# Performance work log

Measured on AMD Instinct MI355X. Metric: run time of the kernel, lower is better.

The kernel has to match this reference:

```python
import jax, jax.numpy as jnp
import numpy as np

D_MODEL = 256
HEADS = 4
HEAD_DIM = D_MODEL // HEADS  # 64
BN_EPS = 1e-5


def conv1(x, W, b):
    # Conv1d kernel_size=1 == per-position linear: x [B,C,N], W [O,C], b [O]
    return jnp.einsum('oc,bcn->bon', W, x) + b[:, None]


def setup_inputs() -> dict:
    key = jax.random.key(0)
    ks = jax.random.split(key, 12)
    B, N, M = 4, 4096, 4096
    s = 0.02
    return {
        'x': jax.random.normal(ks[0], (B, D_MODEL, N), jnp.float32),
        'source': jax.random.normal(ks[1], (B, D_MODEL, M), jnp.float32),
        'pq_w': jax.random.normal(ks[2], (D_MODEL, D_MODEL), jnp.float32) * s,
        'pq_b': jnp.zeros((D_MODEL,), jnp.float32),
        'pk_w': jax.random.normal(ks[3], (D_MODEL, D_MODEL), jnp.float32) * s,
        'pk_b': jnp.zeros((D_MODEL,), jnp.float32),
        'pv_w': jax.random.normal(ks[4], (D_MODEL, D_MODEL), jnp.float32) * s,
        'pv_b': jnp.zeros((D_MODEL,), jnp.float32),
        'merge_w': jax.random.normal(ks[5], (D_MODEL, D_MODEL), jnp.float32) * s,
        'merge_b': jnp.zeros((D_MODEL,), jnp.float32),
        'mlp1_w': jax.random.normal(ks[6], (2 * D_MODEL, 2 * D_MODEL), jnp.float32) * s,
        'mlp1_b': jax.random.normal(ks[7], (2 * D_MODEL,), jnp.float32) * s,
        'bn_gamma': jnp.ones((2 * D_MODEL,), jnp.float32),
        'bn_beta': jnp.zeros((2 * D_MODEL,), jnp.float32),
        'mlp2_w': jax.random.normal(ks[8], (D_MODEL, 2 * D_MODEL), jnp.float32) * s,
        'mlp2_b': jnp.zeros((D_MODEL,), jnp.float32),  # nn.init.constant_(mlp[-1].bias, 0.0)
    }


def reference(x, source, pq_w, pq_b, pk_w, pk_b, pv_w, pv_b,
              merge_w, merge_b, mlp1_w, mlp1_b, bn_gamma, bn_beta,
              mlp2_w, mlp2_b):
    B = x.shape[0]
    # projections; torch view(B, dim, heads, -1): channels split as (head_dim, heads)
    q = conv1(x, pq_w, pq_b).reshape(B, HEAD_DIM, HEADS, -1)       # [B,d,h,N]
    k = conv1(source, pk_w, pk_b).reshape(B, HEAD_DIM, HEADS, -1)  # [B,d,h,M]
    v = conv1(source, pv_w, pv_b).reshape(B, HEAD_DIM, HEADS, -1)
    scores = jnp.einsum('bdhn,bdhm->bhnm', q, k) / (HEAD_DIM ** 0.5)
    prob = jax.nn.softmax(scores, axis=-1)                          # [B,h,N,M]
    attn_out = jnp.einsum('bhnm,bdhm->bdhn', prob, v).reshape(B, D_MODEL, -1)
    message = conv1(attn_out, merge_w, merge_b)                     # [B,D,N]
    # MLP: conv(512->512) + BatchNorm1d (training-mode batch stats) + ReLU + conv(512->256)
    h = conv1(jnp.concatenate([x, message], axis=1), mlp1_w, mlp1_b)  # [B,2D,N]
    mean = jnp.mean(h, axis=(0, 2), keepdims=True)
    var = jnp.var(h, axis=(0, 2), keepdims=True)  # biased, as torch BN uses for normalization
    h = bn_gamma[:, None] * (h - mean) * jax.lax.rsqrt(var + BN_EPS) + bn_beta[:, None]
    h = jax.nn.relu(h)
    return conv1(h, mlp2_w, mlp2_b)
```

## Files before the change

kernel.cpp:

```cpp
#include <hip/hip_runtime.h>
#include <hip/hip_bf16.h>

#define D_MODEL 256
#define HEADS 4
#define HD 64
#define BATCH 4
#define SEQ 4096
#define NPOS (BATCH*SEQ)
#define SCALE_LOG2 0.18033688011112042f
#define MCHUNKS 2

typedef __attribute__((ext_vector_type(4))) float floatx4;
typedef __attribute__((ext_vector_type(8))) short bf16x8;
typedef __attribute__((ext_vector_type(4))) short bf16x4;
typedef __attribute__((ext_vector_type(4))) unsigned short ushortx4;

__device__ __forceinline__ float bf2f(unsigned short b) {
    return __uint_as_float(((unsigned int)b) << 16);
}
__device__ __forceinline__ unsigned short f2bf(float f) {
    unsigned int u = __float_as_uint(f);
    return (unsigned short)((u + 0x7fffu + ((u >> 16) & 1u)) >> 16);
}
__device__ __forceinline__ bf16x4 pack_bf16x4(float a, float b, float c, float d) {
    __hip_bfloat162 lo = __float22bfloat162_rn(float2{a, b});
    __hip_bfloat162 hi = __float22bfloat162_rn(float2{c, d});
    union { __hip_bfloat162 h2[2]; bf16x4 v; } u;
    u.h2[0] = lo; u.h2[1] = hi;
    return u.v;
}
__device__ __forceinline__ bf16x8 pack_bf16x8(floatx4 a, floatx4 b) {
    union { bf16x4 h[2]; bf16x8 v; } u;
    u.h[0] = pack_bf16x4(a[0], a[1], a[2], a[3]);
    u.h[1] = pack_bf16x4(b[0], b[1], b[2], b[3]);
    return u.v;
}
#define MFMA(a,b,c) __builtin_amdgcn_mfma_f32_16x16x32_bf16((a),(b),(c),0,0,0)
#define EXP2(x) __builtin_amdgcn_exp2f(x)

__global__ __launch_bounds__(256) void prep_all(
        const float* __restrict__ pq_w, const float* __restrict__ pk_w,
        const float* __restrict__ pv_w, const float* __restrict__ merge_w,
        const float* __restrict__ mlp1_w, const float* __restrict__ mlp2_w,
        const float* __restrict__ mlp1_b, const float* __restrict__ merge_b,
        const float* __restrict__ x, const float* __restrict__ src,
        unsigned short* __restrict__ wqb, unsigned short* __restrict__ wkb,
        unsigned short* __restrict__ wvb,
        unsigned short* __restrict__ w1b, unsigned short* __restrict__ w2b,
        unsigned short* __restrict__ xT, unsigned short* __restrict__ srcT,
        unsigned short* __restrict__ w1f, float* __restrict__ b1f,
        float* __restrict__ bn_zero)
{
    __shared__ unsigned short smem[64 * 264];
    const int t = threadIdx.x;
    const int bx = blockIdx.x;
    if (bx < 576) {
        int linear = bx * 1024 + t * 4;
        const float* srcW; unsigned short* dst; int off;
        if (linear < 65536)       { srcW = pq_w;   dst = wqb; off = 0; }
        else if (linear < 131072) { srcW = pk_w;   dst = wkb; off = 65536; }
        else if (linear < 196608) { srcW = pv_w;   dst = wvb; off = 131072; }
        else if (linear < 458752) { srcW = mlp1_w; dst = w1b; off = 196608; }
        else                      { srcW = mlp2_w; dst = w2b; off = 458752; }
        int i = linear - off;
        float4 w = *(const float4*)&srcW[i];
        ushortx4 s = { f2bf(w.x), f2bf(w.y), f2bf(w.z), f2bf(w.w) };
        *(ushortx4*)&dst[i] = s;
        return;
    }
    if (bx < 1088) {
        unsigned short (*lT)[264] = (unsigned short (*)[264])smem;
        int z = bx - 576;
        const float* X = (z < 256) ? x : src;
        unsigned short* O = (z < 256) ? xT : srcT;
        int rem = z & 255;
        int b = rem >> 6, n0 = (rem & 63) * 64;
#pragma unroll
        for (int r = 0; r < 16; ++r) {
            int idx = r * 256 + t;
            int ch = idx >> 4, nnq = (idx & 15) * 4;
            float4 v4 = *(const float4*)&X[((size_t)b * 256 + ch) * SEQ + n0 + nnq];
            lT[nnq + 0][ch] = f2bf(v4.x);
            lT[nnq + 1][ch] = f2bf(v4.y);
            lT[nnq + 2][ch] = f2bf(v4.z);
            lT[nnq + 3][ch] = f2bf(v4.w);
        }
        __syncthreads();
#pragma unroll
        for (int r = 0; r < 8; ++r) {
            int idx = r * 256 + t;
            int row = idx >> 5, cg = (idx & 31) * 8;
            *(bf16x8*)&O[((size_t)b * SEQ + n0 + row) * 256 + cg] = *(const bf16x8*)&lT[row][cg];
        }
        return;
    }
    if (bx < 1104) {
        unsigned short (*lA)[40] = (unsigned short (*)[40])smem;
        unsigned short (*lB)[40] = (unsigned short (*)[40])(smem + 64 * 40);
        const int lane = t & 63, wid = t >> 6;
        const int wm = wid >> 1, wn = wid & 1;
        const int lrow = lane & 15, quad = lane >> 4;
        const int fb = bx - 1088;
        const int c0  = (fb & 1) * 128;
        const int o20 = (fb >> 1) * 64;

        floatx4 acc[2][4];
#pragma unroll
        for (int i = 0; i < 2; ++i)
#pragma unroll
            for (int j = 0; j < 4; ++j) acc[i][j] = (floatx4){0.f,0.f,0.f,0.f};

        for (int k0 = 0; k0 < 256; k0 += 32) {
#pragma unroll
            for (int r = 0; r < 2; ++r) {
                int linear = r * 1024 + t * 4;
                int row = linear >> 5, col = linear & 31;
                float4 w = *(const float4*)&mlp1_w[(size_t)(o20 + row) * 512 + 256 + k0 + col];
                ushortx4 s = { f2bf(w.x), f2bf(w.y), f2bf(w.z), f2bf(w.w) };
                *(ushortx4*)&lA[row][col] = s;
            }
#pragma unroll
            for (int r = 0; r < 2; ++r) {
                int linear = r * 256 + t;
                int row = linear >> 2, cg = (linear & 3) * 8;
                int cp = c0 + row;
                int pc = ((cp & 63) << 2) | (cp >> 6);
                unsigned short s[8];
#pragma unroll
                for (int j = 0; j < 8; ++j)
                    s[j] = f2bf(merge_w[(size_t)(k0 + cg + j) * 256 + pc]);
                *(bf16x8*)&lB[row][cg] = *(const bf16x8*)s;
            }
            __syncthreads();
            bf16x8 aF[2], bF[4];
            const int kq = quad * 8;
#pragma unroll
            for (int mt = 0; mt < 2; ++mt)
                aF[mt] = *(const bf16x8*)&lA[wm*32 + mt*16 + lrow][kq];
#pragma unroll
            for (int nt = 0; nt < 4; ++nt)
                bF[nt] = *(const bf16x8*)&lB[wn*64 + nt*16 + lrow][kq];
#pragma unroll
            for (int mt = 0; mt < 2; ++mt)
#pragma unroll
                for (int nt = 0; nt < 4; ++nt)
                    acc[mt][nt] = MFMA(aF[mt], bF[nt], acc[mt][nt]);
            __syncthreads();
        }
#pragma unroll
        for (int nt = 0; nt < 4; ++nt) {
            int cp = c0 + wn*64 + nt*16 + lrow;
#pragma unroll
            for (int mt = 0; mt < 2; ++mt)
#pragma unroll
                for (int j = 0; j < 4; ++j) {
                    int o2 = o20 + wm*32 + mt*16 + quad*4 + j;
                    w1f[(size_t)o2 * 256 + cp] = f2bf(acc[mt][nt][j]);
                }
        }
        return;
    }
    if (bx < 1106) {
        int o2 = (bx - 1104) * 256 + t;
        float s = mlp1_b[o2];
        for (int o = 0; o < 256; ++o)
            s += mlp1_w[(size_t)o2 * 512 + 256 + o] * merge_b[o];
        b1f[o2] = s;
        return;
    }
    *(float4*)&bn_zero[t * 4] = float4{0.f, 0.f, 0.f, 0.f};
}

__global__ __launch_bounds__(256) void proj_qkv_all(
        const unsigned short* __restrict__ Wq, const float* __restrict__ bq,
        const unsigned short* __restrict__ Wk, const float* __restrict__ bk,
        const unsigned short* __restrict__ Wv, const float* __restrict__ bv,
        const unsigned short* __restrict__ xT, const unsigned short* __restrict__ srcT,
        unsigned short* __restrict__ qo, unsigned short* __restrict__ ko,
        unsigned short* __restrict__ vo)
{
    __shared__ unsigned short smem[2][128 * 80];
    unsigned short (*stage)[72] = (unsigned short (*)[72])&smem[0][0];
    unsigned short* stage2 = &smem[0][0];
    const int t = threadIdx.x;
    const int lane = t & 63, wid = t >> 6;
    const int wm = wid >> 1, wn = wid & 1;
    const int lrow = lane & 15, quad = lane >> 4;
    const int mode = blockIdx.x >> 1;
    const int ob = (blockIdx.x & 1) * 128;
    const int n0 = blockIdx.y * 128;
    const int b  = blockIdx.z;
    const unsigned short* W  = (mode == 0) ? Wq : (mode == 1) ? Wk : Wv;
    const float* bias        = (mode == 0) ? bq : (mode == 1) ? bk : bv;
    const unsigned short* XT = (mode == 0) ? xT : srcT;
    unsigned short* out      = (mode == 0) ? qo : (mode == 1) ? ko : vo;

    const int srow[2] = { (0*256 + t) >> 2, (1*256 + t) >> 2 };
    const int scg = (t & 3) * 8;

    floatx4 acc[4][4];
#pragma unroll
    for (int i = 0; i < 4; ++i)
#pragma unroll
        for (int j = 0; j < 4; ++j) acc[i][j] = (floatx4){0.f,0.f,0.f,0.f};

    bf16x8 rW[2], rX[2];
#pragma unroll
    for (int r = 0; r < 2; ++r) {
        rW[r] = *(const bf16x8*)&W[(size_t)(ob + srow[r]) * 256 + scg];
        rX[r] = *(const bf16x8*)&XT[((size_t)b * SEQ + n0 + srow[r]) * 256 + scg];
    }
#pragma unroll
    for (int r = 0; r < 2; ++r) {
        *(bf16x8*)&smem[0][srow[r]*40 + scg]           = rW[r];
        *(bf16x8*)&smem[0][128*40 + srow[r]*40 + scg]  = rX[r];
    }
    __syncthreads();

    int p = 0;
    for (int kc = 0; kc < 8; ++kc) {
        const bool pre = (kc + 1 < 8);
        if (pre) {
            const int k1 = (kc + 1) * 32;
#pragma unroll
            for (int r = 0; r < 2; ++r) {
                rW[r] = *(const bf16x8*)&W[(size_t)(ob + srow[r]) * 256 + k1 + scg];
                rX[r] = *(const bf16x8*)&XT[((size_t)b * SEQ + n0 + srow[r]) * 256 + k1 + scg];
            }
        }
        bf16x8 aF[4], bF[4];
        const int kq = quad * 8;
#pragma unroll
        for (int mt = 0; mt < 4; ++mt)
            aF[mt] = *(const bf16x8*)&smem[p][(wm*64 + mt*16 + lrow)*40 + kq];
#pragma unroll
        for (int nt = 0; nt < 4; ++nt)
            bF[nt] = *(const bf16x8*)&smem[p][128*40 + (wn*64 + nt*16 + lrow)*40 + kq];
#pragma unroll
        for (int mt = 0; mt < 4; ++mt)
#pragma unroll
            for (int nt = 0; nt < 4; ++nt)
                acc[mt][nt] = MFMA(aF[mt], bF[nt], acc[mt][nt]);
        if (pre) {
#pragma unroll
            for (int r = 0; r < 2; ++r) {
                *(bf16x8*)&smem[p^1][srow[r]*40 + scg]          = rW[r];
                *(bf16x8*)&smem[p^1][128*40 + srow[r]*40 + scg] = rX[r];
            }
        }
        __syncthreads();
        p ^= 1;
    }
    const float osc = (mode == 0) ? SCALE_LOG2 : 1.0f;
    if (mode == 2) {
        for (int half = 0; half < 2; ++half) {
            __syncthreads();
            if (wm == half) {
#pragma unroll
                for (int mt = 0; mt < 4; ++mt)
#pragma unroll
                    for (int j = 0; j < 4; ++j) {
                        int ol = mt*16 + quad*4 + j;
                        float bvv = bias[ob + half*64 + ol];
#pragma unroll
                        for (int nt = 0; nt < 4; ++nt) {
                            int n = wn*64 + nt*16 + lrow;
                            stage2[ol*132 + n] = f2bf(acc[mt][nt][j] + bvv);
                        }
                    }
            }
            __syncthreads();
#pragma unroll
            for (int i = 0; i < 4; ++i) {
                int c = i * 256 + t;
                int row = c >> 4, sub = c & 15;
                int o = ob + half*64 + row;
                int d = o >> 2, h = o & 3;
                *(bf16x8*)&out[((size_t)(b*HEADS + h) * HD + d) * SEQ + n0 + sub*8] =
                    *(const bf16x8*)&stage2[row*132 + sub*8];
            }
        }
        return;
    }
    for (int half = 0; half < 2; ++half) {
        __syncthreads();
        if (wm == half) {
#pragma unroll
            for (int mt = 0; mt < 4; ++mt)
#pragma unroll
                for (int j = 0; j < 4; ++j) {
                    int o = ob + half*64 + mt*16 + quad*4 + j;
                    float bvv = bias[o];
                    int col = j*16 + mt*4 + quad;
#pragma unroll
                    for (int nt = 0; nt < 4; ++nt) {
                        int n = wn*64 + nt*16 + lrow;
                        stage[n][col] = f2bf((acc[mt][nt][j] + bvv) * osc);
                    }
                }
        }
        __syncthreads();
#pragma unroll
        for (int i = 0; i < 4; ++i) {
            int c = i * 256 + t;
            int n = c >> 3, h = (c >> 1) & 3, sub = c & 1;
            bf16x8 val = *(const bf16x8*)&stage[n][h*16 + sub*8];
            int d0 = (ob >> 2) + half*16 + sub*8;
            *(bf16x8*)&out[((size_t)(b*HEADS + h) * SEQ + n0 + n) * HD + d0] = val;
        }
    }
}

__global__ __launch_bounds__(256, 2) void flash_attn(
        const unsigned short* __restrict__ q,
        const unsigned short* __restrict__ k,
        const unsigned short* __restrict__ v,
        unsigned short* __restrict__ poO, float* __restrict__ pol)
{
    __shared__ unsigned short smem[2][9216];
    const int t = threadIdx.x, lane = t & 63, wid = t >> 6;
    const int lrow = lane & 15, quad = lane >> 4;
    const int bc = blockIdx.x, qt = blockIdx.y;
    const int bh = bc & 15, chunk = bc >> 4;
    const int hb = (bh & 3) * BATCH + (bh >> 2);
    const int r0 = qt * 256 + wid * 64;

    bf16x8 qf[4][2];
#pragma unroll
    for (int nh = 0; nh < 4; ++nh) {
        const size_t base = ((size_t)bh * SEQ + r0 + nh*16 + lrow) * HD;
        qf[nh][0] = *(const bf16x8*)&q[base + quad * 8];
        qf[nh][1] = *(const bf16x8*)&q[base + 32 + quad * 8];
    }
    bf16x8 ones;
#pragma unroll
    for (int i = 0; i < 8; ++i) ones[i] = (short)0x3F80;
    int mmv[2], cgv[2], krv[2];
#pragma unroll
    for (int r = 0; r < 2; ++r) {
        int linear = r * 256 + t;
        int mm = linear >> 3, cg = (linear & 7) * 8;
        int c2 = mm >> 5, mp = mm & 31;
        mmv[r] = mm; cgv[r] = cg;
        krv[r] = (c2 << 5) + ((mp & 4) << 2) + ((mp >> 3) << 2) + (mp & 3);
    }
    const size_t kbase = ((size_t)bh * SEQ + chunk * (SEQ/MCHUNKS));
    const size_t vbase = (size_t)bh * HD;
    const int moff = chunk * (SEQ/MCHUNKS);
    const int NIT = SEQ / MCHUNKS / 64;

    floatx4 oacc[4][4], oaccL[4];
#pragma unroll
    for (int nh = 0; nh < 4; ++nh) {
        oaccL[nh] = (floatx4){0.f,0.f,0.f,0.f};
#pragma unroll
        for (int i = 0; i < 4; ++i) oacc[nh][i] = (floatx4){0.f,0.f,0.f,0.f};
    }

    {
        bf16x8 pk[2], pv[2];
#pragma unroll
        for (int r = 0; r < 2; ++r) {
            pk[r] = *(const bf16x8*)&k[(kbase + mmv[r]) * HD + cgv[r]];
            pv[r] = *(const bf16x8*)&v[(vbase + mmv[r]) * SEQ + moff + cgv[r]];
        }
#pragma unroll
        for (int r = 0; r < 2; ++r) {
            *(bf16x8*)&smem[0][krv[r]*72 + cgv[r]]        = pk[r];
            *(bf16x8*)&smem[0][4608 + mmv[r]*72 + cgv[r]] = pv[r];
        }
    }
    __syncthreads();

    int p = 0;
#pragma unroll 1
    for (int it = 0; it < NIT; ++it) {
        bf16x8 pk[2], pv[2];
        const bool pre = (it + 1 < NIT);
        if (pre) {
            const int m1 = (it + 1) * 64;
#pragma unroll
            for (int r = 0; r < 2; ++r) {
                pk[r] = *(const bf16x8*)&k[(kbase + m1 + mmv[r]) * HD + cgv[r]];
                pv[r] = *(const bf16x8*)&v[(vbase + mmv[r]) * SEQ + moff + m1 + cgv[r]];
            }
        }
        const unsigned short* lS = smem[p];

#pragma unroll
        for (int c2 = 0; c2 < 2; ++c2) {
            floatx4 sa[2][4];
#pragma unroll
            for (int AB = 0; AB < 2; ++AB)
#pragma unroll
                for (int nh = 0; nh < 4; ++nh)
                    sa[AB][nh] = (floatx4){0.f,0.f,0.f,0.f};
            __builtin_amdgcn_s_setprio(1);
#pragma unroll
            for (int AB = 0; AB < 2; ++AB) {
#pragma unroll
                for (int kc = 0; kc < 2; ++kc) {
                    bf16x8 kf = *(const bf16x8*)&lS[(c2*32 + AB*16 + lrow)*72 + kc*32 + quad*8];
#pragma unroll
                    for (int nh = 0; nh < 4; ++nh)
                        sa[AB][nh] = MFMA(kf, qf[nh][kc], sa[AB][nh]);
                }
            }
            __builtin_amdgcn_s_setprio(0);
            bf16x8 pf8[4];
#pragma unroll
            for (int nh = 0; nh < 4; ++nh) {
                floatx4 ea, eb;
#pragma unroll
                for (int i = 0; i < 4; ++i) { ea[i] = EXP2(sa[0][nh][i]); eb[i] = EXP2(sa[1][nh][i]); }
                pf8[nh] = pack_bf16x8(ea, eb);
            }
            __builtin_amdgcn_s_setprio(1);
#pragma unroll
            for (int nh = 0; nh < 4; ++nh)
                oaccL[nh] = MFMA(ones, pf8[nh], oaccL[nh]);
#pragma unroll
            for (int dt = 0; dt < 4; ++dt) {
                bf16x8 vf = *(const bf16x8*)&lS[4608 + (dt*16 + lrow)*72 + c2*32 + quad*8];
#pragma unroll
                for (int nh = 0; nh < 4; ++nh)
                    oacc[nh][dt] = MFMA(vf, pf8[nh], oacc[nh][dt]);
            }
            __builtin_amdgcn_s_setprio(0);
        }
        if (pre) {
#pragma unroll
            for (int r = 0; r < 2; ++r) {
                *(bf16x8*)&smem[p^1][krv[r]*72 + cgv[r]]        = pk[r];
                *(bf16x8*)&smem[p^1][4608 + mmv[r]*72 + cgv[r]] = pv[r];
            }
        }
        __syncthreads();
        p ^= 1;
    }
    const size_t prow = (size_t)(chunk*16 + hb) * SEQ + qt * 256;
    if (lane < 16) {
#pragma unroll
        for (int nh = 0; nh < 4; ++nh)
            pol[prow + wid*64 + nh*16 + lrow] = oaccL[nh][0];
    }
    unsigned short* stB = (unsigned short*)&smem[0][0];
#pragma unroll
    for (int nh = 0; nh < 4; ++nh)
#pragma unroll
        for (int dt = 0; dt < 4; ++dt) {
            bf16x4 pv4 = pack_bf16x4(oacc[nh][dt][0], oacc[nh][dt][1],
                                     oacc[nh][dt][2], oacc[nh][dt][3]);
            *(bf16x4*)&stB[(wid*64 + nh*16 + lrow)*72 + dt*16 + quad*4] = pv4;
        }
    __syncthreads();
#pragma unroll
    for (int i = 0; i < 8; ++i) {
        int c = i * 256 + t;
        int row = c >> 3, sub = c & 7;
        *(bf16x8*)&poO[(prow + row) * HD + sub*8] = *(const bf16x8*)&stB[row*72 + sub*8];
    }
}

__global__ __launch_bounds__(256) void gemm_mlp1(
        const unsigned short* __restrict__ xT, const unsigned short* __restrict__ poO,
        const float* __restrict__ pol,
        const unsigned short* __restrict__ w1b, const unsigned short* __restrict__ w1f,
        const float* __restrict__ b1f, unsigned short* __restrict__ h1,
        float* __restrict__ sums, float* __restrict__ sumsq)
{
    __shared__ unsigned short lA[2][64][40];
    __shared__ unsigned short lB[2][128][40];
    __shared__ float sInv[256];
    const int t = threadIdx.x;
    const int lane = t & 63, wid = t >> 6;
    const int wm = wid >> 1, wn = wid & 1;
    const int lrow = lane & 15, quad = lane >> 4;
    const int o0 = blockIdx.x * 128;
    const int p0 = blockIdx.y * 64;
    const int b = p0 >> 12, n0 = p0 & (SEQ - 1);
    const size_t CH = (size_t)16 * SEQ * HD;

    {
        int h = t >> 6, nn = t & 63;
        int hb = h * BATCH + b;
        float l = 0.f;
#pragma unroll
        for (int c = 0; c < MCHUNKS; ++c)
            l += pol[((size_t)(c*16 + hb)) * SEQ + n0 + nn];
        sInv[t] = 1.0f / l;
    }
    __syncthreads();

    const int arow = t >> 2, acg = (t & 3) * 8;
    const int brow[2] = { (0*256 + t) >> 2, (1*256 + t) >> 2 };

    floatx4 acc[2][4];
#pragma unroll
    for (int i = 0; i < 2; ++i)
#pragma unroll
        for (int j = 0; j < 4; ++j) acc[i][j] = (floatx4){0.f,0.f,0.f,0.f};

    bf16x8 rA, rB[2];
    auto load_tile = [&](int k0) {
        if (k0 < 256) {
            rA = *(const bf16x8*)&xT[(size_t)(p0 + arow) * 256 + k0 + acg];
#pragma unroll
            for (int r = 0; r < 2; ++r)
                rB[r] = *(const bf16x8*)&w1b[(size_t)(o0 + brow[r]) * 512 + k0 + acg];
        } else {
            const int kk2 = k0 - 256;
            const int h = kk2 >> 6, d0 = kk2 & 63, hb = h * BATCH + b;
            const unsigned short* bse = &poO[((size_t)hb * SEQ + n0 + arow) * HD + d0 + acg];
            float inv = sInv[h*64 + arow];
            float fs[8];
#pragma unroll
            for (int i = 0; i < 8; ++i) fs[i] = 0.f;
#pragma unroll
            for (int c = 0; c < MCHUNKS; ++c) {
                bf16x8 a = *(const bf16x8*)(bse + (size_t)c * CH);
#pragma unroll
                for (int i = 0; i < 8; ++i)
                    fs[i] += bf2f((unsigned short)a[i]);
            }
            unsigned short res[8];
#pragma unroll
            for (int i = 0; i < 8; ++i)
                res[i] = f2bf(fs[i] * inv);
            rA = *(const bf16x8*)res;
#pragma unroll
            for (int r = 0; r < 2; ++r)
                rB[r] = *(const bf16x8*)&w1f[(size_t)(o0 + brow[r]) * 256 + kk2 + acg];
        }
    };

    load_tile(0);
    *(bf16x8*)&lA[0][arow][acg] = rA;
#pragma unroll
    for (int r = 0; r < 2; ++r) *(bf16x8*)&lB[0][brow[r]][acg] = rB[r];
    __syncthreads();

    int p = 0;
    for (int kc = 0; kc < 16; ++kc) {
        const bool pre = (kc + 1 < 16);
        if (pre) load_tile((kc + 1) * 32);
        bf16x8 aF[2], bF[4];
        const int kq = quad * 8;
#pragma unroll
        for (int mt = 0; mt < 2; ++mt)
            aF[mt] = *(const bf16x8*)&lA[p][wm*32 + mt*16 + lrow][kq];
#pragma unroll
        for (int nt = 0; nt < 4; ++nt)
            bF[nt] = *(const bf16x8*)&lB[p][wn*64 + nt*16 + lrow][kq];
#pragma unroll
        for (int mt = 0; mt < 2; ++mt)
#pragma unroll
            for (int nt = 0; nt < 4; ++nt)
                acc[mt][nt] = MFMA(aF[mt], bF[nt], acc[mt][nt]);
        if (pre) {
            *(bf16x8*)&lA[p^1][arow][acg] = rA;
#pragma unroll
            for (int r = 0; r < 2; ++r) *(bf16x8*)&lB[p^1][brow[r]][acg] = rB[r];
        }
        __syncthreads();
        p ^= 1;
    }
#pragma unroll
    for (int nt = 0; nt < 4; ++nt) {
        int o = o0 + wn*64 + nt*16 + lrow;
        float bvv = b1f[o];
        float s = 0.f, qs = 0.f;
#pragma unroll
        for (int mt = 0; mt < 2; ++mt)
#pragma unroll
            for (int j = 0; j < 4; ++j) {
                int pos = p0 + wm*32 + mt*16 + quad*4 + j;
                float val = acc[mt][nt][j] + bvv;
                h1[(size_t)pos * 512 + o] = f2bf(val);
                s += val; qs += val * val;
            }
        s  += __shfl_xor(s, 16);  s  += __shfl_xor(s, 32);
        qs += __shfl_xor(qs, 16); qs += __shfl_xor(qs, 32);
        if (lane < 16) {
            atomicAdd(&sums[o], s);
            atomicAdd(&sumsq[o], qs);
        }
    }
}

__global__ __launch_bounds__(256) void gemm_mlp2(
        const unsigned short* __restrict__ W2, const unsigned short* __restrict__ h1,
        const float* __restrict__ bias,
        const float* __restrict__ sums, const float* __restrict__ sumsq,
        const float* __restrict__ gamma, const float* __restrict__ beta,
        float* __restrict__ out)
{
    __shared__ unsigned short lA[2][128][40];
    __shared__ unsigned short lB[2][64][40];
    __shared__ float sSc[512], sSh[512];
    const int t = threadIdx.x;
    const int lane = t & 63, wid = t >> 6;
    const int wm = wid >> 1, wn = wid & 1;
    const int lrow = lane & 15, quad = lane >> 4;
    const int o0 = blockIdx.x * 128;
    const int p0 = blockIdx.y * 64;

#pragma unroll
    for (int cc = 0; cc < 2; ++cc) {
        int c = cc * 256 + t;
        float mean = sums[c] * (1.0f / NPOS);
        float var  = sumsq[c] * (1.0f / NPOS) - mean * mean;
        float sc = gamma[c] * rsqrtf(var + 1e-5f);
        sSc[c] = sc;
        sSh[c] = beta[c] - mean * sc;
    }
    __syncthreads();

    const int arow[2] = { (0*256 + t) >> 2, (1*256 + t) >> 2 };
    const int acg = (t & 3) * 8;
    const int brow = t >> 2;

    floatx4 acc[4][2];
#pragma unroll
    for (int i = 0; i < 4; ++i)
#pragma unroll
        for (int j = 0; j < 2; ++j) acc[i][j] = (floatx4){0.f,0.f,0.f,0.f};

    bf16x8 rW[2], rH;
    auto load_tile = [&](int k0) {
#pragma unroll
        for (int r = 0; r < 2; ++r)
            rW[r] = *(const bf16x8*)&W2[(size_t)(o0 + arow[r]) * 512 + k0 + acg];
        bf16x8 hv = *(const bf16x8*)&h1[(size_t)(p0 + brow) * 512 + k0 + acg];
        unsigned short res[8];
#pragma unroll
        for (int i = 0; i < 8; ++i) {
            int c = k0 + acg + i;
            float f = bf2f((unsigned short)hv[i]);
            f = fmaxf(f * sSc[c] + sSh[c], 0.f);
            res[i] = f2bf(f);
        }
        rH = *(const bf16x8*)res;
    };

    load_tile(0);
#pragma unroll
    for (int r = 0; r < 2; ++r) *(bf16x8*)&lA[0][arow[r]][acg] = rW[r];
    *(bf16x8*)&lB[0][brow][acg] = rH;
    __syncthreads();

    int p = 0;
    for (int kc = 0; kc < 16; ++kc) {
        const bool pre = (kc + 1 < 16);
        if (pre) load_tile((kc + 1) * 32);
        bf16x8 aF[4], bF[2];
        const int kq = quad * 8;
#pragma unroll
        for (int mt = 0; mt < 4; ++mt)
            aF[mt] = *(const bf16x8*)&lA[p][wm*64 + mt*16 + lrow][kq];
#pragma unroll
        for (int nt = 0; nt < 2; ++nt)
            bF[nt] = *(const bf16x8*)&lB[p][wn*32 + nt*16 + lrow][kq];
#pragma unroll
        for (int mt = 0; mt < 4; ++mt)
#pragma unroll
            for (int nt = 0; nt < 2; ++nt)
                acc[mt][nt] = MFMA(aF[mt], bF[nt], acc[mt][nt]);
        if (pre) {
#pragma unroll
            for (int r = 0; r < 2; ++r) *(bf16x8*)&lA[p^1][arow[r]][acg] = rW[r];
            *(bf16x8*)&lB[p^1][brow][acg] = rH;
        }
        __syncthreads();
        p ^= 1;
    }
#pragma unroll
    for (int mt = 0; mt < 4; ++mt)
#pragma unroll
        for (int j = 0; j < 4; ++j) {
            int o = o0 + wm*64 + mt*16 + quad*4 + j;
            float bvv = bias[o];
#pragma unroll
            for (int nt = 0; nt < 2; ++nt) {
                int pos = p0 + wn*32 + nt*16 + lrow;
                int b = pos >> 12, n = pos & (SEQ - 1);
                out[((size_t)b * D_MODEL + o) * SEQ + n] = acc[mt][nt][j] + bvv;
            }
        }
}

extern "C" void kernel_launch(void* const* d_in, const int* in_sizes, int n_in,
                              void* d_out, int out_size, void* d_ws, size_t ws_size,
                              hipStream_t stream)
{
    (void)in_sizes; (void)n_in; (void)out_size; (void)ws_size;
    const float* x        = (const float*)d_in[0];
    const float* source   = (const float*)d_in[1];
    const float* pq_w     = (const float*)d_in[2];
    const float* pq_b     = (const float*)d_in[3];
    const float* pk_w     = (const float*)d_in[4];
    const float* pk_b     = (const float*)d_in[5];
    const float* pv_w     = (const float*)d_in[6];
    const float* pv_b     = (const float*)d_in[7];
    const float* merge_w  = (const float*)d_in[8];
    const float* merge_b  = (const float*)d_in[9];
    const float* mlp1_w   = (const float*)d_in[10];
    const float* mlp1_b   = (const float*)d_in[11];
    const float* bn_gamma = (const float*)d_in[12];
    const float* bn_beta  = (const float*)d_in[13];
    const float* mlp2_w   = (const float*)d_in[14];
    const float* mlp2_b   = (const float*)d_in[15];
    float* out = (float*)d_out;

    char* ws = (char*)d_ws;
    const size_t MB = 1ull << 20;
    unsigned short* xT   = (unsigned short*)(ws);
    unsigned short* srcT = (unsigned short*)(ws + 8*MB);
    unsigned short* q    = (unsigned short*)(ws + 16*MB);
    unsigned short* kk   = (unsigned short*)(ws + 24*MB);
    unsigned short* v    = (unsigned short*)(ws + 32*MB);
    unsigned short* poO  = (unsigned short*)(ws + 40*MB);
    unsigned short* h1   = (unsigned short*)(ws + 16*MB);
    float* pol = (float*)(ws + 72*MB);
    unsigned short* wqb = (unsigned short*)(ws + 73*MB);
    unsigned short* wkb = wqb + 65536;
    unsigned short* wvb = wkb + 65536;
    unsigned short* w1b = wvb + 65536;
    unsigned short* w2b = w1b + 262144;
    unsigned short* w1f = w2b + 131072;
    float* b1f = (float*)(w1f + 131072);
    float* bn_sum = b1f + 512;
    float* bn_sumsq = bn_sum + 512;

    prep_all<<<dim3(1107), 256, 0, stream>>>(
        pq_w, pk_w, pv_w, merge_w, mlp1_w, mlp2_w, mlp1_b, merge_b, x, source,
        wqb, wkb, wvb, w1b, w2b, xT, srcT, w1f, b1f, bn_sum);
    proj_qkv_all<<<dim3(6, SEQ/128, BATCH), 256, 0, stream>>>(
        wqb, pq_b, wkb, pk_b, wvb, pv_b, xT, srcT, q, kk, v);
    flash_attn<<<dim3(16*MCHUNKS, SEQ/256), 256, 0, stream>>>(q, kk, v, poO, pol);
    gemm_mlp1<<<dim3(4, NPOS/64), 256, 0, stream>>>(
        xT, poO, pol, w1b, w1f, b1f, h1, bn_sum, bn_sumsq);
    gemm_mlp2<<<dim3(2, NPOS/64), 256, 0, stream>>>(
        w2b, h1, mlp2_b, bn_sum, bn_sumsq, bn_gamma, bn_beta, out);
}
```

Measured before the change: 243.4 us.

## Enlarge mlp1 GEMM tiles, interleave attention chunk partials, parallelize bias fold

gemm_mlp1 now uses 512-thread blocks with 128x256 output tiles instead of 64x128. This quarters the number of blocks, increases operand reuse from shared memory, and halves the BN-stat atomics by reducing across warps in shared memory first. The flash-attention partial outputs and row sums are now stored with the chunk index innermost, so mlp1 reads both chunks contiguously. The bias-folding prep block is spread over 16 blocks with a shuffle reduction instead of 2 blocks doing serial 256-length dot products. The larger tiles cost more registers and LDS per block, which may lower occupancy, and there are fewer blocks (256) to fill the GPU.

```diff
diff --git a/kernel.cpp b/kernel.cpp
--- a/kernel.cpp
+++ b/kernel.cpp
@@ -160,12 +160,15 @@
         }
         return;
     }
-    if (bx < 1106) {
-        int o2 = (bx - 1104) * 256 + t;
-        float s = mlp1_b[o2];
-        for (int o = 0; o < 256; ++o)
-            s += mlp1_w[(size_t)o2 * 512 + 256 + o] * merge_b[o];
-        b1f[o2] = s;
+    if (bx < 1120) {
+        int o2 = (bx - 1104) * 32 + (t >> 3);
+        int kl = t & 7;
+        float s = 0.f;
+#pragma unroll
+        for (int o = 0; o < 32; ++o)
+            s += mlp1_w[(size_t)o2 * 512 + 256 + kl*32 + o] * merge_b[kl*32 + o];
+        s += __shfl_xor(s, 1); s += __shfl_xor(s, 2); s += __shfl_xor(s, 4);
+        if (kl == 0) b1f[o2] = mlp1_b[o2] + s;
         return;
     }
     *(float4*)&bn_zero[t * 4] = float4{0.f, 0.f, 0.f, 0.f};
@@ -438,11 +441,11 @@
         __syncthreads();
         p ^= 1;
     }
-    const size_t prow = (size_t)(chunk*16 + hb) * SEQ + qt * 256;
+    const size_t nb = (size_t)hb * SEQ + qt * 256;
     if (lane < 16) {
 #pragma unroll
         for (int nh = 0; nh < 4; ++nh)
-            pol[prow + wid*64 + nh*16 + lrow] = oaccL[nh][0];
+            pol[(nb + wid*64 + nh*16 + lrow) * MCHUNKS + chunk] = oaccL[nh][0];
     }
     unsigned short* stB = (unsigned short*)&smem[0][0];
 #pragma unroll
@@ -458,46 +461,44 @@
     for (int i = 0; i < 8; ++i) {
         int c = i * 256 + t;
         int row = c >> 3, sub = c & 7;
-        *(bf16x8*)&poO[(prow + row) * HD + sub*8] = *(const bf16x8*)&stB[row*72 + sub*8];
-    }
-}
-
-__global__ __launch_bounds__(256) void gemm_mlp1(
+        *(bf16x8*)&poO[((nb + row) * MCHUNKS + chunk) * HD + sub*8] =
+            *(const bf16x8*)&stB[row*72 + sub*8];
+    }
+}
+
+__global__ __launch_bounds__(512) void gemm_mlp1(
         const unsigned short* __restrict__ xT, const unsigned short* __restrict__ poO,
         const float* __restrict__ pol,
         const unsigned short* __restrict__ w1b, const unsigned short* __restrict__ w1f,
         const float* __restrict__ b1f, unsigned short* __restrict__ h1,
         float* __restrict__ sums, float* __restrict__ sumsq)
 {
-    __shared__ unsigned short lA[2][64][40];
-    __shared__ unsigned short lB[2][128][40];
-    __shared__ float sInv[256];
+    __shared__ unsigned short lA[2][128][40];
+    __shared__ unsigned short lB[2][256][40];
+    __shared__ float sInv[512];
+    __shared__ float sRed[4][4][16][2];
     const int t = threadIdx.x;
     const int lane = t & 63, wid = t >> 6;
-    const int wm = wid >> 1, wn = wid & 1;
+    const int wp = wid >> 2, wo = wid & 3;
     const int lrow = lane & 15, quad = lane >> 4;
-    const int o0 = blockIdx.x * 128;
-    const int p0 = blockIdx.y * 64;
+    const int o0 = blockIdx.x * 256;
+    const int p0 = blockIdx.y * 128;
     const int b = p0 >> 12, n0 = p0 & (SEQ - 1);
-    const size_t CH = (size_t)16 * SEQ * HD;
 
     {
-        int h = t >> 6, nn = t & 63;
+        int h = t >> 7, nn = t & 127;
         int hb = h * BATCH + b;
-        float l = 0.f;
-#pragma unroll
-        for (int c = 0; c < MCHUNKS; ++c)
-            l += pol[((size_t)(c*16 + hb)) * SEQ + n0 + nn];
-        sInv[t] = 1.0f / l;
+        float2 l2 = *(const float2*)&pol[((size_t)hb * SEQ + n0 + nn) * MCHUNKS];
+        sInv[t] = 1.0f / (l2.x + l2.y);
     }
     __syncthreads();
 
     const int arow = t >> 2, acg = (t & 3) * 8;
-    const int brow[2] = { (0*256 + t) >> 2, (1*256 + t) >> 2 };
-
-    floatx4 acc[2][4];
-#pragma unroll
-    for (int i = 0; i < 2; ++i)
+    const int brow[2] = { (0*512 + t) >> 2, (1*512 + t) >> 2 };
+
+    floatx4 acc[4][4];
+#pragma unroll
+    for (int i = 0; i < 4; ++i)
 #pragma unroll
         for (int j = 0; j < 4; ++j) acc[i][j] = (floatx4){0.f,0.f,0.f,0.f};
 
@@ -511,22 +512,15 @@
         } else {
             const int kk2 = k0 - 256;
             const int h = kk2 >> 6, d0 = kk2 & 63, hb = h * BATCH + b;
-            const unsigned short* bse = &poO[((size_t)hb * SEQ + n0 + arow) * HD + d0 + acg];
-            float inv = sInv[h*64 + arow];
-            float fs[8];
-#pragma unroll
-            for (int i = 0; i < 8; ++i) fs[i] = 0.f;
-#pragma unroll
-            for (int c = 0; c < MCHUNKS; ++c) {
-                bf16x8 a = *(const bf16x8*)(bse + (size_t)c * CH);
-#pragma unroll
-                for (int i = 0; i < 8; ++i)
-                    fs[i] += bf2f((unsigned short)a[i]);
-            }
+            const unsigned short* bse =
+                &poO[(((size_t)hb * SEQ + n0 + arow) * MCHUNKS) * HD + d0 + acg];
+            float inv = sInv[h*128 + arow];
+            bf16x8 a0 = *(const bf16x8*)bse;
+            bf16x8 a1 = *(const bf16x8*)(bse + HD);
             unsigned short res[8];
 #pragma unroll
             for (int i = 0; i < 8; ++i)
-                res[i] = f2bf(fs[i] * inv);
+                res[i] = f2bf((bf2f((unsigned short)a0[i]) + bf2f((unsigned short)a1[i])) * inv);
             rA = *(const bf16x8*)res;
 #pragma unroll
             for (int r = 0; r < 2; ++r)
@@ -544,16 +538,16 @@
     for (int kc = 0; kc < 16; ++kc) {
         const bool pre = (kc + 1 < 16);
         if (pre) load_tile((kc + 1) * 32);
-        bf16x8 aF[2], bF[4];
+        bf16x8 aF[4], bF[4];
         const int kq = quad * 8;
 #pragma unroll
-        for (int mt = 0; mt < 2; ++mt)
-            aF[mt] = *(const bf16x8*)&lA[p][wm*32 + mt*16 + lrow][kq];
+        for (int mt = 0; mt < 4; ++mt)
+            aF[mt] = *(const bf16x8*)&lA[p][wp*64 + mt*16 + lrow][kq];
 #pragma unroll
         for (int nt = 0; nt < 4; ++nt)
-            bF[nt] = *(const bf16x8*)&lB[p][wn*64 + nt*16 + lrow][kq];
-#pragma unroll
-        for (int mt = 0; mt < 2; ++mt)
+            bF[nt] = *(const bf16x8*)&lB[p][wo*64 + nt*16 + lrow][kq];
+#pragma unroll
+        for (int mt = 0; mt < 4; ++mt)
 #pragma unroll
             for (int nt = 0; nt < 4; ++nt)
                 acc[mt][nt] = MFMA(aF[mt], bF[nt], acc[mt][nt]);
@@ -567,23 +561,28 @@
     }
 #pragma unroll
     for (int nt = 0; nt < 4; ++nt) {
-        int o = o0 + wn*64 + nt*16 + lrow;
+        int o = o0 + wo*64 + nt*16 + lrow;
         float bvv = b1f[o];
         float s = 0.f, qs = 0.f;
 #pragma unroll
-        for (int mt = 0; mt < 2; ++mt)
+        for (int mt = 0; mt < 4; ++mt)
 #pragma unroll
             for (int j = 0; j < 4; ++j) {
-                int pos = p0 + wm*32 + mt*16 + quad*4 + j;
+                int pos = p0 + wp*64 + mt*16 + quad*4 + j;
                 float val = acc[mt][nt][j] + bvv;
                 h1[(size_t)pos * 512 + o] = f2bf(val);
                 s += val; qs += val * val;
             }
         s  += __shfl_xor(s, 16);  s  += __shfl_xor(s, 32);
         qs += __shfl_xor(qs, 16); qs += __shfl_xor(qs, 32);
-        if (lane < 16) {
-            atomicAdd(&sums[o], s);
-            atomicAdd(&sumsq[o], qs);
+        if (wp == 1 && lane < 16) {
+            sRed[wo][nt][lrow][0] = s;
+            sRed[wo][nt][lrow][1] = qs;
+        }
+        __syncthreads();
+        if (wp == 0 && lane < 16) {
+            atomicAdd(&sums[o],  s  + sRed[wo][nt][lrow][0]);
+            atomicAdd(&sumsq[o], qs + sRed[wo][nt][lrow][1]);
         }
     }
 }
@@ -732,13 +731,13 @@
     float* bn_sum = b1f + 512;
     float* bn_sumsq = bn_sum + 512;
 
-    prep_all<<<dim3(1107), 256, 0, stream>>>(
+    prep_all<<<dim3(1121), 256, 0, stream>>>(
         pq_w, pk_w, pv_w, merge_w, mlp1_w, mlp2_w, mlp1_b, merge_b, x, source,
         wqb, wkb, wvb, w1b, w2b, xT, srcT, w1f, b1f, bn_sum);
     proj_qkv_all<<<dim3(6, SEQ/128, BATCH), 256, 0, stream>>>(
         wqb, pq_b, wkb, pk_b, wvb, pv_b, xT, srcT, q, kk, v);
     flash_attn<<<dim3(16*MCHUNKS, SEQ/256), 256, 0, stream>>>(q, kk, v, poO, pol);
-    gemm_mlp1<<<dim3(4, NPOS/64), 256, 0, stream>>>(
+    gemm_mlp1<<<dim3(2, NPOS/128), 512, 0, stream>>>(
         xT, poO, pol, w1b, w1f, b1f, h1, bn_sum, bn_sumsq);
     gemm_mlp2<<<dim3(2, NPOS/64), 256, 0, stream>>>(
         w2b, h1, mlp2_b, bn_sum, bn_sumsq, bn_gamma, bn_beta, out);
```

Result: faster. 238.1 us (-2.2%).
